# Kernel tuning notes

Measured on AMD Instinct MI355X. Metric: run time of the kernel, lower is better.

Reference implementation:

```python
import jax, jax.numpy as jnp
import numpy as np

DIM, HEADS, KV_HEADS = 1024, 16, 4
B, T = 1, 4096
HEAD_DIM = DIM // HEADS           # 64
KV_DIM = DIM // (HEADS // KV_HEADS)  # 256
SCALE = HEAD_DIM ** -0.5


def setup_inputs() -> dict:
    key = jax.random.key(0)
    ks = jax.random.split(key, 9)
    s = lambda fan_in: fan_in ** -0.5
    return {
        "x": jax.random.normal(ks[0], (B, T, DIM), jnp.float32),
        "mask": jnp.tril(jnp.ones((1, 1, T, T), jnp.bool_)),  # causal
        "q_w": jax.random.normal(ks[1], (DIM, DIM), jnp.float32) * s(DIM),
        "q_b": jnp.zeros((DIM,), jnp.float32),
        "k_w": jax.random.normal(ks[2], (KV_DIM, DIM), jnp.float32) * s(DIM),
        "k_b": jnp.zeros((KV_DIM,), jnp.float32),
        "v_w": jax.random.normal(ks[3], (KV_DIM, DIM), jnp.float32) * s(DIM),
        "v_b": jnp.zeros((KV_DIM,), jnp.float32),
        "o_w": jax.random.normal(ks[4], (DIM, DIM), jnp.float32) * s(DIM),
        "o_b": jnp.zeros((DIM,), jnp.float32),
    }


def reference(x, mask, q_w, q_b, k_w, k_b, v_w, v_b, o_w, o_b):
    b, t, d = x.shape
    g = HEADS // KV_HEADS  # query heads per kv head
    # projections (torch Linear: x @ W^T + b)
    q = (x @ q_w.T + q_b).reshape(b, t, HEADS, HEAD_DIM).transpose(0, 2, 1, 3)      # [B,H,T,hd]
    k = (x @ k_w.T + k_b).reshape(b, t, KV_HEADS, HEAD_DIM).transpose(0, 2, 1, 3)   # [B,Hk,T,hd]
    v = (x @ v_w.T + v_b).reshape(b, t, KV_HEADS, HEAD_DIM).transpose(0, 2, 1, 3)   # [B,Hk,T,hd]
    # GQA: group query heads over shared kv heads
    qg = q.reshape(b, KV_HEADS, g, t, HEAD_DIM)                                     # [B,Hk,g,T,hd]
    scores = jnp.einsum('bkgtd,bksd->bkgts', qg, k) * SCALE                         # [B,Hk,g,T,T]
    scores = jnp.where(mask[:, :, None, :, :], scores, -1e9)
    attn = jax.nn.softmax(scores, axis=-1)  # dropout is identity in eval mode
    out = jnp.einsum('bkgts,bksd->bkgtd', attn, v)                                  # [B,Hk,g,T,hd]
    out = out.reshape(b, HEADS, t, HEAD_DIM).transpose(0, 2, 1, 3).reshape(b, t, d)
    out = out @ o_w.T + o_b
    return out, k, v  # (output, new kv cache)
```

## Files before the change

### kernel.cpp

```cpp
#include <hip/hip_runtime.h>
#include <hip/hip_bf16.h>
#include <stdint.h>

typedef __bf16 bf16;
typedef __bf16 bf16x8 __attribute__((ext_vector_type(8)));
typedef float  f32x4 __attribute__((ext_vector_type(4)));

#define SEQ   4096
#define DIM_  1024
#define HD_   64
#define NEG_BIG (-30000.0f)

__device__ __forceinline__ bf16x8 cvt8(const float* p) {
    f32x4 a = *(const f32x4*)p, b = *(const f32x4*)(p + 4);
    bf16x8 r;
    r[0]=(bf16)a[0]; r[1]=(bf16)a[1]; r[2]=(bf16)a[2]; r[3]=(bf16)a[3];
    r[4]=(bf16)b[0]; r[5]=(bf16)b[1]; r[6]=(bf16)b[2]; r[7]=(bf16)b[3];
    return r;
}

__device__ __forceinline__ bf16x8 pack8(f32x4 a, f32x4 b) {
    bf16x8 r;
    r[0]=(bf16)a[0]; r[1]=(bf16)a[1]; r[2]=(bf16)a[2]; r[3]=(bf16)a[3];
    r[4]=(bf16)b[0]; r[5]=(bf16)b[1]; r[6]=(bf16)b[2]; r[7]=(bf16)b[3];
    return r;
}

template<int MODE>
__global__ __launch_bounds__(256)
void gemm_bt(const void* __restrict__ Av,
             const float* __restrict__ B0, const float* __restrict__ b0,
             const float* __restrict__ B1, const float* __restrict__ b1,
             const float* __restrict__ B2, const float* __restrict__ b2,
             float* __restrict__ C0, float* __restrict__ C1, float* __restrict__ C2,
             bf16* __restrict__ Qbf)
{
    const int K = 1024;
    const int tid  = threadIdx.x;
    const int lane = tid & 63, wave = tid >> 6;
    const int qd = lane >> 4, ln = lane & 15;
    const int wm = (wave & 1) * 64, wn = (wave >> 1) * 64;
    const int m0 = blockIdx.x * 128, n0 = blockIdx.y * 128;

    const float* Bp; const float* bias;
    if (MODE == 1) {
        if (n0 < 1024)      { Bp = B0 + (size_t)n0 * K;        bias = b0 + n0; }
        else if (n0 < 1280) { Bp = B1 + (size_t)(n0-1024) * K; bias = b1 + (n0-1024); }
        else                { Bp = B2 + (size_t)(n0-1280) * K; bias = b2 + (n0-1280); }
    } else                  { Bp = B0 + (size_t)n0 * K;        bias = b0 + n0; }

    __shared__ bf16 As[128*32];
    __shared__ bf16 Bs[128*32];

    f32x4 acc[4][4] = {};

    for (int k0 = 0; k0 < K; k0 += 32) {
        bf16x8 ra[2], rb[2];
        #pragma unroll
        for (int i = 0; i < 2; ++i) {
            int s   = i*256 + tid;
            int row = s >> 2, ch = s & 3;
            if (MODE == 0)
                ra[i] = *(const bf16x8*)((const bf16*)Av + (size_t)(m0+row)*K + k0 + ch*8);
            else
                ra[i] = cvt8((const float*)Av + (size_t)(m0+row)*K + k0 + ch*8);
            rb[i] = cvt8(Bp + (size_t)row*K + k0 + ch*8);
        }
        __syncthreads();
        #pragma unroll
        for (int i = 0; i < 2; ++i) {
            int s   = i*256 + tid;
            int row = s >> 2, ch = s & 3;
            *(bf16x8*)(As + row*32 + ch*8) = ra[i];
            *(bf16x8*)(Bs + row*32 + ch*8) = rb[i];
        }
        __syncthreads();

        bf16x8 af[4], bg[4];
        #pragma unroll
        for (int i = 0; i < 4; ++i)
            af[i] = *(const bf16x8*)(As + (wm + i*16 + ln)*32 + qd*8);
        #pragma unroll
        for (int j = 0; j < 4; ++j)
            bg[j] = *(const bf16x8*)(Bs + (wn + j*16 + ln)*32 + qd*8);

        #pragma unroll
        for (int i = 0; i < 4; ++i)
            #pragma unroll
            for (int j = 0; j < 4; ++j)
                acc[i][j] = __builtin_amdgcn_mfma_f32_16x16x32_bf16(af[i], bg[j], acc[i][j], 0, 0, 0);
    }

    #pragma unroll
    for (int i = 0; i < 4; ++i) {
        #pragma unroll
        for (int j = 0; j < 4; ++j) {
            int colg = n0 + wn + j*16 + ln;
            float bv = bias[wn + j*16 + ln];
            #pragma unroll
            for (int r = 0; r < 4; ++r) {
                int rowg = m0 + wm + i*16 + qd*4 + r;
                float v = acc[i][j][r] + bv;
                if (MODE == 0) {
                    C0[(size_t)rowg*1024 + colg] = v;
                } else if (colg < 1024) {
                    Qbf[(size_t)rowg*1024 + colg] = (bf16)(v * 0.125f);
                } else if (colg < 1280) {
                    int c2 = colg - 1024;
                    C1[(size_t)(c2 >> 6)*(SEQ*HD_) + (size_t)rowg*HD_ + (c2 & 63)] = v;
                } else {
                    int c2 = colg - 1280;
                    C2[(size_t)(c2 >> 6)*(SEQ*HD_) + (size_t)rowg*HD_ + (c2 & 63)] = v;
                }
            }
        }
    }
}

__global__ __launch_bounds__(256)
void kv_cvt(const float* __restrict__ kout, const float* __restrict__ vout,
            bf16* __restrict__ k_bf, bf16* __restrict__ vT_bf)
{
    const int b   = blockIdx.x;
    const int kvh = b >> 6, tb = b & 63;
    const int tid = threadIdx.x;

    __shared__ float T[64*65];

    const float* Ksrc = kout + ((size_t)kvh*SEQ + tb*64) * HD_;
    const float* Vsrc = vout + ((size_t)kvh*SEQ + tb*64) * HD_;

    #pragma unroll
    for (int i = 0; i < 2; ++i) {
        int s = i*256 + tid;
        int r = s >> 3, c = s & 7;
        *(bf16x8*)(k_bf + ((size_t)kvh*SEQ + tb*64 + r)*HD_ + c*8)
            = cvt8(Ksrc + (size_t)r*HD_ + c*8);
        f32x4 va = *(const f32x4*)(Vsrc + (size_t)r*HD_ + c*8);
        f32x4 vb = *(const f32x4*)(Vsrc + (size_t)r*HD_ + c*8 + 4);
        #pragma unroll
        for (int e = 0; e < 4; ++e) T[(c*8 + e)*65 + r]     = va[e];
        #pragma unroll
        for (int e = 0; e < 4; ++e) T[(c*8 + 4 + e)*65 + r] = vb[e];
    }
    __syncthreads();
    #pragma unroll
    for (int i = 0; i < 2; ++i) {
        int s = i*256 + tid;
        int d = s >> 3, c = s & 7;
        f32x4 a = *(const f32x4*)(T + d*65 + c*8);
        f32x4 bq = *(const f32x4*)(T + d*65 + c*8 + 4);
        *(bf16x8*)(vT_bf + ((size_t)kvh*HD_ + d)*SEQ + tb*64 + c*8) = pack8(a, bq);
    }
}

__global__ __launch_bounds__(256)
void attn_fwd(const bf16* __restrict__ Q, const bf16* __restrict__ Kc,
              const bf16* __restrict__ VT, bf16* __restrict__ att)
{
    const int bid  = blockIdx.x;
    const int head = bid & 15;
    const int mt   = 63 - (bid >> 4);
    const int qb   = mt * 64;
    const int kvh  = head >> 2;

    const int tid = threadIdx.x, lane = tid & 63, wave = tid >> 6;
    const int qd = lane >> 4, ln = lane & 15;
    const int rw0 = qb + wave * 16;

    __shared__ bf16 Ks[64*72];
    __shared__ bf16 Vt[64*72];
    __shared__ bf16 Ps[4][16*72];

    const bf16* Kbase = Kc + (size_t)kvh * SEQ * HD_;
    const bf16* Vbase = VT + (size_t)kvh * HD_ * SEQ;

    bf16x8 aq[2];
    #pragma unroll
    for (int ks = 0; ks < 2; ++ks)
        aq[ks] = *(const bf16x8*)(Q + (size_t)(rw0 + ln)*DIM_ + head*HD_ + ks*32 + qd*8);

    f32x4 o[4] = {};
    float l_p[4] = {0.f, 0.f, 0.f, 0.f};

    const float LOG2E = 1.4426950408889634f;
    const float C16   = 16.0f * LOG2E;
    const int nkt = mt + 1;

    for (int kt = 0; kt < nkt; ++kt) {
        const int kb = kt * 64;

        bf16x8 rk[2], rv[2];
        #pragma unroll
        for (int i = 0; i < 2; ++i) {
            int s = i*256 + tid;
            int r8 = s >> 3, ch = s & 7;
            rk[i] = *(const bf16x8*)(Kbase + (size_t)(kb + r8)*HD_ + ch*8);
            rv[i] = *(const bf16x8*)(Vbase + (size_t)r8*SEQ + kb + ch*8);
        }
        __syncthreads();
        #pragma unroll
        for (int i = 0; i < 2; ++i) {
            int s = i*256 + tid;
            int r8 = s >> 3, ch = s & 7;
            *(bf16x8*)(Ks + r8*72 + ch*8) = rk[i];
            *(bf16x8*)(Vt + r8*72 + ch*8) = rv[i];
        }
        __syncthreads();

        f32x4 S[4] = {};
        #pragma unroll
        for (int ks = 0; ks < 2; ++ks) {
            bf16x8 bk[4];
            #pragma unroll
            for (int nf = 0; nf < 4; ++nf)
                bk[nf] = *(const bf16x8*)(Ks + (nf*16 + ln)*72 + ks*32 + qd*8);
            #pragma unroll
            for (int nf = 0; nf < 4; ++nf)
                S[nf] = __builtin_amdgcn_mfma_f32_16x16x32_bf16(aq[ks], bk[nf], S[nf], 0, 0, 0);
        }

        if (kt == nkt - 1) {
            #pragma unroll
            for (int nf = 0; nf < 4; ++nf) {
                int col = kb + nf*16 + ln;
                #pragma unroll
                for (int r = 0; r < 4; ++r) {
                    int row = rw0 + qd*4 + r;
                    if (col > row) S[nf][r] = NEG_BIG;
                }
            }
        }

        bf16* Pw = &Ps[wave][0];
        #pragma unroll
        for (int r = 0; r < 4; ++r) {
            #pragma unroll
            for (int nf = 0; nf < 4; ++nf) {
                float p = exp2f(S[nf][r] * LOG2E - C16);
                l_p[r] += p;
                Pw[(qd*4 + r)*72 + nf*16 + ln] = (bf16)p;
            }
        }
        asm volatile("s_waitcnt lgkmcnt(0)" ::: "memory");

        #pragma unroll
        for (int ks = 0; ks < 2; ++ks) {
            bf16x8 bv[4];
            #pragma unroll
            for (int nf = 0; nf < 4; ++nf)
                bv[nf] = *(const bf16x8*)(Vt + (nf*16 + ln)*72 + ks*32 + qd*8);
            bf16x8 ap = *(const bf16x8*)(&Ps[wave][ln*72 + ks*32 + qd*8]);
            #pragma unroll
            for (int nf = 0; nf < 4; ++nf)
                o[nf] = __builtin_amdgcn_mfma_f32_16x16x32_bf16(ap, bv[nf], o[nf], 0, 0, 0);
        }
    }

    #pragma unroll
    for (int r = 0; r < 4; ++r) {
        float l = l_p[r];
        l += __shfl_xor(l, 1);
        l += __shfl_xor(l, 2);
        l += __shfl_xor(l, 4);
        l += __shfl_xor(l, 8);
        float inv = 1.0f / l;
        int trow = rw0 + qd*4 + r;
        #pragma unroll
        for (int nf = 0; nf < 4; ++nf)
            att[(size_t)trow*DIM_ + head*HD_ + nf*16 + ln] = (bf16)(o[nf][r] * inv);
    }
}

extern "C" void kernel_launch(void* const* d_in, const int* in_sizes, int n_in,
                              void* d_out, int out_size, void* d_ws, size_t ws_size,
                              hipStream_t stream)
{
    const float* x  = (const float*)d_in[0];
    const float* qw = (const float*)d_in[2];
    const float* qb = (const float*)d_in[3];
    const float* kw = (const float*)d_in[4];
    const float* kb = (const float*)d_in[5];
    const float* vw = (const float*)d_in[6];
    const float* vb = (const float*)d_in[7];
    const float* ow = (const float*)d_in[8];
    const float* ob = (const float*)d_in[9];

    float* out  = (float*)d_out;
    float* kout = out  + (size_t)SEQ * DIM_;
    float* vout = kout + (size_t)4 * SEQ * HD_;

    bf16* q_bf  = (bf16*)d_out;
    bf16* k_bf  = q_bf + (size_t)SEQ * DIM_;
    bf16* vT_bf = k_bf + (size_t)4 * SEQ * HD_;
    bf16* att   = (bf16*)d_ws;

    gemm_bt<1><<<dim3(32, 12), 256, 0, stream>>>(x, qw, qb, kw, kb, vw, vb,
                                                 nullptr, kout, vout, q_bf);
    kv_cvt<<<dim3(256), 256, 0, stream>>>(kout, vout, k_bf, vT_bf);
    attn_fwd<<<dim3(1024), 256, 0, stream>>>(q_bf, k_bf, vT_bf, att);
    gemm_bt<0><<<dim3(32, 8), 256, 0, stream>>>(att, ow, ob, nullptr, nullptr,
                                                nullptr, nullptr, out, nullptr, nullptr,
                                                nullptr);
}
```

Measured before the change: 282.6 us.

## Split-K the KV and output projections with atomic accumulation to fill more CUs

The fused QKV GEMM becomes a 1D grid of 512 blocks. Q tiles run the full K range, while the K/V tiles are split into two K halves that atomically add into fp32 buffers pre-filled with bias by a new init kernel. The output projection likewise uses split-K of two over 512 blocks, with atomics into an output pre-initialised with the bias. The aim is better CU occupancy on the small GEMMs, at the cost of two extra init launches, extra memory traffic for the bias fills, and float atomics whose summation order is nondeterministic.

```diff
diff --git a/kernel.cpp b/kernel.cpp
--- a/kernel.cpp
+++ b/kernel.cpp
@@ -26,45 +26,71 @@
     return r;
 }
 
-template<int MODE>
-__global__ __launch_bounds__(256)
-void gemm_bt(const void* __restrict__ Av,
-             const float* __restrict__ B0, const float* __restrict__ b0,
-             const float* __restrict__ B1, const float* __restrict__ b1,
-             const float* __restrict__ B2, const float* __restrict__ b2,
-             float* __restrict__ C0, float* __restrict__ C1, float* __restrict__ C2,
-             bf16* __restrict__ Qbf)
+__global__ __launch_bounds__(256)
+void init_kv(const float* __restrict__ kb, const float* __restrict__ vb,
+             float* __restrict__ kout, float* __restrict__ vout)
+{
+    int i  = blockIdx.x * 256 + threadIdx.x;
+    int e8 = i * 8;
+    int kvh = e8 >> 18;
+    int d   = e8 & 63;
+    *(f32x4*)(kout + e8)     = *(const f32x4*)(kb + kvh*64 + d);
+    *(f32x4*)(kout + e8 + 4) = *(const f32x4*)(kb + kvh*64 + d + 4);
+    *(f32x4*)(vout + e8)     = *(const f32x4*)(vb + kvh*64 + d);
+    *(f32x4*)(vout + e8 + 4) = *(const f32x4*)(vb + kvh*64 + d + 4);
+}
+
+__global__ __launch_bounds__(256)
+void init_out(const float* __restrict__ ob, float* __restrict__ out)
+{
+    int i  = blockIdx.x * 256 + threadIdx.x;
+    int e8 = i * 8;
+    int c  = e8 & 1023;
+    *(f32x4*)(out + e8)     = *(const f32x4*)(ob + c);
+    *(f32x4*)(out + e8 + 4) = *(const f32x4*)(ob + c + 4);
+}
+
+__global__ __launch_bounds__(256)
+void gemm_qkv(const float* __restrict__ x,
+              const float* __restrict__ qw, const float* __restrict__ qb,
+              const float* __restrict__ kw, const float* __restrict__ vw,
+              float* __restrict__ kout, float* __restrict__ vout,
+              bf16* __restrict__ q_bf)
 {
     const int K = 1024;
+    const int id = blockIdx.x;
+    int m0, n0, k_beg, k_end;
+    bool isQ;
+    if (id < 256) {
+        isQ = true;  m0 = (id >> 3) * 128; n0 = (id & 7) * 128;
+        k_beg = 0; k_end = 1024;
+    } else {
+        int t = id - 256;
+        isQ = false; m0 = (t >> 3) * 128; n0 = 1024 + ((t >> 1) & 3) * 128;
+        k_beg = (t & 1) * 512; k_end = k_beg + 512;
+    }
+    const float* Bp = isQ ? qw + (size_t)n0 * K
+                    : (n0 < 1280 ? kw + (size_t)(n0 - 1024) * K
+                                 : vw + (size_t)(n0 - 1280) * K);
+
     const int tid  = threadIdx.x;
     const int lane = tid & 63, wave = tid >> 6;
     const int qd = lane >> 4, ln = lane & 15;
     const int wm = (wave & 1) * 64, wn = (wave >> 1) * 64;
-    const int m0 = blockIdx.x * 128, n0 = blockIdx.y * 128;
-
-    const float* Bp; const float* bias;
-    if (MODE == 1) {
-        if (n0 < 1024)      { Bp = B0 + (size_t)n0 * K;        bias = b0 + n0; }
-        else if (n0 < 1280) { Bp = B1 + (size_t)(n0-1024) * K; bias = b1 + (n0-1024); }
-        else                { Bp = B2 + (size_t)(n0-1280) * K; bias = b2 + (n0-1280); }
-    } else                  { Bp = B0 + (size_t)n0 * K;        bias = b0 + n0; }
 
     __shared__ bf16 As[128*32];
     __shared__ bf16 Bs[128*32];
 
     f32x4 acc[4][4] = {};
 
-    for (int k0 = 0; k0 < K; k0 += 32) {
+    for (int k0 = k_beg; k0 < k_end; k0 += 32) {
         bf16x8 ra[2], rb[2];
         #pragma unroll
         for (int i = 0; i < 2; ++i) {
             int s   = i*256 + tid;
             int row = s >> 2, ch = s & 3;
-            if (MODE == 0)
-                ra[i] = *(const bf16x8*)((const bf16*)Av + (size_t)(m0+row)*K + k0 + ch*8);
-            else
-                ra[i] = cvt8((const float*)Av + (size_t)(m0+row)*K + k0 + ch*8);
-            rb[i] = cvt8(Bp + (size_t)row*K + k0 + ch*8);
+            ra[i] = cvt8(x  + (size_t)(m0+row)*K + k0 + ch*8);
+            rb[i] = cvt8(Bp + (size_t)row*K      + k0 + ch*8);
         }
         __syncthreads();
         #pragma unroll
@@ -96,25 +122,90 @@
         #pragma unroll
         for (int j = 0; j < 4; ++j) {
             int colg = n0 + wn + j*16 + ln;
-            float bv = bias[wn + j*16 + ln];
             #pragma unroll
             for (int r = 0; r < 4; ++r) {
                 int rowg = m0 + wm + i*16 + qd*4 + r;
-                float v = acc[i][j][r] + bv;
-                if (MODE == 0) {
-                    C0[(size_t)rowg*1024 + colg] = v;
-                } else if (colg < 1024) {
-                    Qbf[(size_t)rowg*1024 + colg] = (bf16)(v * 0.125f);
+                float v = acc[i][j][r];
+                if (isQ) {
+                    q_bf[(size_t)rowg*1024 + colg] = (bf16)((v + qb[colg]) * 0.125f);
                 } else if (colg < 1280) {
                     int c2 = colg - 1024;
-                    C1[(size_t)(c2 >> 6)*(SEQ*HD_) + (size_t)rowg*HD_ + (c2 & 63)] = v;
+                    atomicAdd(kout + (size_t)(c2 >> 6)*(SEQ*HD_) + (size_t)rowg*HD_ + (c2 & 63), v);
                 } else {
                     int c2 = colg - 1280;
-                    C2[(size_t)(c2 >> 6)*(SEQ*HD_) + (size_t)rowg*HD_ + (c2 & 63)] = v;
+                    atomicAdd(vout + (size_t)(c2 >> 6)*(SEQ*HD_) + (size_t)rowg*HD_ + (c2 & 63), v);
                 }
             }
         }
     }
+}
+
+__global__ __launch_bounds__(256)
+void gemm_o(const bf16* __restrict__ att, const float* __restrict__ ow,
+            float* __restrict__ out)
+{
+    const int K = 1024;
+    const int id = blockIdx.x;
+    const int m0 = (id >> 4) * 128;
+    const int n0 = ((id >> 1) & 7) * 128;
+    const int k_beg = (id & 1) * 512, k_end = k_beg + 512;
+
+    const int tid  = threadIdx.x;
+    const int lane = tid & 63, wave = tid >> 6;
+    const int qd = lane >> 4, ln = lane & 15;
+    const int wm = (wave & 1) * 64, wn = (wave >> 1) * 64;
+    const float* Bp = ow + (size_t)n0 * K;
+
+    __shared__ bf16 As[128*32];
+    __shared__ bf16 Bs[128*32];
+
+    f32x4 acc[4][4] = {};
+
+    for (int k0 = k_beg; k0 < k_end; k0 += 32) {
+        bf16x8 ra[2], rb[2];
+        #pragma unroll
+        for (int i = 0; i < 2; ++i) {
+            int s   = i*256 + tid;
+            int row = s >> 2, ch = s & 3;
+            ra[i] = *(const bf16x8*)(att + (size_t)(m0+row)*K + k0 + ch*8);
+            rb[i] = cvt8(Bp + (size_t)row*K + k0 + ch*8);
+        }
+        __syncthreads();
+        #pragma unroll
+        for (int i = 0; i < 2; ++i) {
+            int s   = i*256 + tid;
+            int row = s >> 2, ch = s & 3;
+            *(bf16x8*)(As + row*32 + ch*8) = ra[i];
+            *(bf16x8*)(Bs + row*32 + ch*8) = rb[i];
+        }
+        __syncthreads();
+
+        bf16x8 af[4], bg[4];
+        #pragma unroll
+        for (int i = 0; i < 4; ++i)
+            af[i] = *(const bf16x8*)(As + (wm + i*16 + ln)*32 + qd*8);
+        #pragma unroll
+        for (int j = 0; j < 4; ++j)
+            bg[j] = *(const bf16x8*)(Bs + (wn + j*16 + ln)*32 + qd*8);
+
+        #pragma unroll
+        for (int i = 0; i < 4; ++i)
+            #pragma unroll
+            for (int j = 0; j < 4; ++j)
+                acc[i][j] = __builtin_amdgcn_mfma_f32_16x16x32_bf16(af[i], bg[j], acc[i][j], 0, 0, 0);
+    }
+
+    #pragma unroll
+    for (int i = 0; i < 4; ++i)
+        #pragma unroll
+        for (int j = 0; j < 4; ++j) {
+            int colg = n0 + wn + j*16 + ln;
+            #pragma unroll
+            for (int r = 0; r < 4; ++r) {
+                int rowg = m0 + wm + i*16 + qd*4 + r;
+                atomicAdd(out + (size_t)rowg*1024 + colg, acc[i][j][r]);
+            }
+        }
 }
 
 __global__ __launch_bounds__(256)
@@ -148,7 +239,7 @@
     for (int i = 0; i < 2; ++i) {
         int s = i*256 + tid;
         int d = s >> 3, c = s & 7;
-        f32x4 a = *(const f32x4*)(T + d*65 + c*8);
+        f32x4 a  = *(const f32x4*)(T + d*65 + c*8);
         f32x4 bq = *(const f32x4*)(T + d*65 + c*8 + 4);
         *(bf16x8*)(vT_bf + ((size_t)kvh*HD_ + d)*SEQ + tb*64 + c*8) = pack8(a, bq);
     }
@@ -295,11 +386,11 @@
     bf16* vT_bf = k_bf + (size_t)4 * SEQ * HD_;
     bf16* att   = (bf16*)d_ws;
 
-    gemm_bt<1><<<dim3(32, 12), 256, 0, stream>>>(x, qw, qb, kw, kb, vw, vb,
-                                                 nullptr, kout, vout, q_bf);
+    init_kv<<<dim3(512), 256, 0, stream>>>(kb, vb, kout, vout);
+    gemm_qkv<<<dim3(512), 256, 0, stream>>>(x, qw, qb, kw, vw,
+                                            kout, vout, q_bf);
     kv_cvt<<<dim3(256), 256, 0, stream>>>(kout, vout, k_bf, vT_bf);
     attn_fwd<<<dim3(1024), 256, 0, stream>>>(q_bf, k_bf, vT_bf, att);
-    gemm_bt<0><<<dim3(32, 8), 256, 0, stream>>>(att, ow, ob, nullptr, nullptr,
-                                                nullptr, nullptr, out, nullptr, nullptr,
-                                                nullptr);
-}
+    init_out<<<dim3(2048), 256, 0, stream>>>(ob, out);
+    gemm_o<<<dim3(512), 256, 0, stream>>>(att, ow, out);
+}
```

New measurement: 311.7 us. 10.3% more time.
